# Performance work log

Measured on AMD Instinct MI355X. Metric: run time of the kernel, lower is better.

Reference implementation:

```python
import jax, jax.numpy as jnp
import numpy as np

N_NODES = 50000
N_EDGES = 1_600_000
FEAT, HIDDEN, NUM_CLASS = 128, 128, 64


def setup_inputs() -> dict:
    key = jax.random.key(0)
    k1, k2, k3, k4, k5 = jax.random.split(key, 5)
    h = jax.random.normal(k1, (N_NODES, FEAT), dtype=jnp.float32)
    edge_index = jax.random.randint(k2, (2, N_EDGES), 0, N_NODES, dtype=jnp.int32)
    # Glorot-ish init for the three GraphConv weights (bias=False)
    W1 = jax.random.normal(k3, (FEAT, HIDDEN), dtype=jnp.float32) * (1.0 / np.sqrt(FEAT))
    W2 = jax.random.normal(k4, (HIDDEN, HIDDEN), dtype=jnp.float32) * (1.0 / np.sqrt(HIDDEN))
    W3 = jax.random.normal(k5, (HIDDEN, NUM_CLASS), dtype=jnp.float32) * (1.0 / np.sqrt(HIDDEN))
    return {"h": h, "edge_index": edge_index, "W1": W1, "W2": W2, "W3": W3}


def _gcn_layer(h, W, src, dst, out_isqrt, in_isqrt, n_nodes):
    # DGL GraphConv, norm='both', bias=False: relu( D_in^{-1/2} A D_out^{-1/2} h W )
    h = h * out_isqrt[:, None]          # scale source features
    h = h @ W                            # dense projection (order-invariant)
    agg = jax.ops.segment_sum(h[src], dst, num_segments=n_nodes)  # SpMM aggregation
    agg = agg * in_isqrt[:, None]
    return jax.nn.relu(agg)


def reference(h, edge_index, W1, W2, W3):
    src, dst = edge_index[0], edge_index[1]
    ones = jnp.ones(src.shape[0], dtype=h.dtype)
    out_deg = jax.ops.segment_sum(ones, src, num_segments=N_NODES)
    in_deg = jax.ops.segment_sum(ones, dst, num_segments=N_NODES)
    out_isqrt = jnp.clip(out_deg, 1.0, None) ** -0.5
    in_isqrt = jnp.clip(in_deg, 1.0, None) ** -0.5
    h = _gcn_layer(h, W1, src, dst, out_isqrt, in_isqrt, N_NODES)
    h = _gcn_layer(h, W2, src, dst, out_isqrt, in_isqrt, N_NODES)
    h = _gcn_layer(h, W3, src, dst, out_isqrt, in_isqrt, N_NODES)
    return h
```

## Files before the change

kernel.cpp:

```cpp
#include <hip/hip_runtime.h>

#define N_NODES 50000
#define N_EDGES 1600000
#define FEAT 128
#define HIDDEN 128
#define NUM_CLASS 64

#define NBUCK 782
#define EPB 2048
#define NBLK 782
#define SCAP 2560
#define AGG_NBN 3125
#define GEMM_BLOCKS 782

#define HISTROW 50048
#define HISTW (HISTROW / 4)
#define NSHAD 128
#define HIST_EPB 12500

typedef _Float16 h8 __attribute__((ext_vector_type(8)));
typedef _Float16 h4 __attribute__((ext_vector_type(4)));
typedef float f32x4 __attribute__((ext_vector_type(4)));

__global__ __launch_bounds__(256) void passA_kernel(const int* __restrict__ ei,
                                                    unsigned* __restrict__ priv,
                                                    int* __restrict__ localoff,
                                                    int* __restrict__ Cmat) {
    __shared__ int cnt[1024];
    __shared__ int base[1024];
    __shared__ int cur[1024];
    __shared__ int tmp[256];
    __shared__ unsigned sorted[EPB];
    const int t = threadIdx.x;
    const int blk = blockIdx.x;
    for (int i = t; i < 1024; i += 256) cnt[i] = 0;
    __syncthreads();

    const int ebase = blk * EPB;
    unsigned packed[8];
    int bk[8];
#pragma unroll
    for (int j = 0; j < 8; ++j) {
        const int e = ebase + t + j * 256;
        if (e < N_EDGES) {
            const unsigned s = (unsigned)ei[e];
            const unsigned d = (unsigned)ei[N_EDGES + e];
            bk[j] = (int)(d >> 6);
            packed[j] = s | ((d & 63u) << 16) | ((d >> 6) << 22);
            atomicAdd(&cnt[bk[j]], 1);
        } else bk[j] = -1;
    }
    __syncthreads();

    const int c0 = cnt[4*t], c1 = cnt[4*t+1], c2 = cnt[4*t+2], c3 = cnt[4*t+3];
    const int s = c0 + c1 + c2 + c3;
    tmp[t] = s;
    __syncthreads();
    for (int off = 1; off < 256; off <<= 1) {
        int v = (t >= off) ? tmp[t - off] : 0;
        __syncthreads();
        tmp[t] += v;
        __syncthreads();
    }
    const int excl = tmp[t] - s;
    base[4*t] = excl;            cur[4*t] = excl;
    base[4*t+1] = excl+c0;       cur[4*t+1] = excl+c0;
    base[4*t+2] = excl+c0+c1;    cur[4*t+2] = excl+c0+c1;
    base[4*t+3] = excl+c0+c1+c2; cur[4*t+3] = excl+c0+c1+c2;
    __syncthreads();

    for (int b = t; b < NBUCK; b += 256) {
        localoff[(size_t)blk * NBUCK + b] = base[b];
        Cmat[(size_t)blk * NBUCK + b] = cnt[b];
    }
#pragma unroll
    for (int j = 0; j < 8; ++j)
        if (bk[j] >= 0) {
            const int pos = atomicAdd(&cur[bk[j]], 1);
            sorted[pos] = packed[j];
        }
    __syncthreads();
    const int total = min(EPB, N_EDGES - ebase);
    for (int i = t; i < total; i += 256) priv[(size_t)blk * EPB + i] = sorted[i];
}

__global__ __launch_bounds__(256) void hist8_kernel(const int* __restrict__ ei,
                                                    unsigned* __restrict__ hist8) {
    __shared__ unsigned hh[HISTW];
    const int t = threadIdx.x;
    for (int i = t; i < HISTW; i += 256) hh[i] = 0;
    __syncthreads();
    const int base = blockIdx.x * HIST_EPB;
    for (int j = t; j < HIST_EPB; j += 256) {
        const unsigned s = (unsigned)ei[base + j];
        atomicAdd(&hh[s >> 2], 1u << ((s & 3u) * 8u));
    }
    __syncthreads();
    unsigned* dst = hist8 + (size_t)blockIdx.x * HISTW;
    for (int i = t; i < HISTW; i += 256) dst[i] = hh[i];
}

__global__ __launch_bounds__(256) void scales8_kernel(const unsigned* __restrict__ hist8,
                                                      float* __restrict__ out_isqrt) {
    const int w = blockIdx.x * 256 + threadIdx.x;
    if (w >= HISTW) return;
    unsigned s0 = 0, s1 = 0, s2 = 0, s3 = 0;
    for (int b = 0; b < NSHAD; ++b) {
        const unsigned u = hist8[(size_t)b * HISTW + w];
        s0 += u & 255u; s1 += (u >> 8) & 255u; s2 += (u >> 16) & 255u; s3 += u >> 24;
    }
    const int n = w * 4;
    if (n < N_NODES)     out_isqrt[n]     = rsqrtf((float)(s0 < 1 ? 1 : s0));
    if (n + 1 < N_NODES) out_isqrt[n + 1] = rsqrtf((float)(s1 < 1 ? 1 : s1));
    if (n + 2 < N_NODES) out_isqrt[n + 2] = rsqrtf((float)(s2 < 1 ? 1 : s2));
    if (n + 3 < N_NODES) out_isqrt[n + 3] = rsqrtf((float)(s3 < 1 ? 1 : s3));
}

__global__ __launch_bounds__(256) void btotal_kernel(const int* __restrict__ Cmat,
                                                     int* __restrict__ total) {
    __shared__ int red[256];
    const int b = blockIdx.x;
    const int t = threadIdx.x;
    int s = 0;
    for (int blk = t; blk < NBLK; blk += 256) s += Cmat[(size_t)blk * NBUCK + b];
    red[t] = s;
    __syncthreads();
    for (int off = 128; off > 0; off >>= 1) {
        if (t < off) red[t] += red[t + off];
        __syncthreads();
    }
    if (t == 0) total[b] = red[0];
}

__global__ __launch_bounds__(256) void bscan2_kernel(const int* __restrict__ total,
                                                     int* __restrict__ csr_base,
                                                     int* __restrict__ row_off) {
    __shared__ int tt[1024];
    __shared__ int tmp[256];
    const int t = threadIdx.x;
    for (int i = t; i < 1024; i += 256) tt[i] = (i < NBUCK) ? total[i] : 0;
    __syncthreads();
    const int c0 = tt[4*t], c1 = tt[4*t+1], c2 = tt[4*t+2], c3 = tt[4*t+3];
    const int s = c0 + c1 + c2 + c3;
    tmp[t] = s;
    __syncthreads();
    for (int off = 1; off < 256; off <<= 1) {
        int v = (t >= off) ? tmp[t - off] : 0;
        __syncthreads();
        tmp[t] += v;
        __syncthreads();
    }
    const int excl = tmp[t] - s;
    if (4*t < NBUCK)   csr_base[4*t]   = excl;
    if (4*t+1 < NBUCK) csr_base[4*t+1] = excl + c0;
    if (4*t+2 < NBUCK) csr_base[4*t+2] = excl + c0 + c1;
    if (4*t+3 < NBUCK) csr_base[4*t+3] = excl + c0 + c1 + c2;
    if (t == 0) { csr_base[NBUCK] = N_EDGES; row_off[N_NODES] = N_EDGES; }
}

__global__ __launch_bounds__(256) void csr2_kernel(const int* __restrict__ localoff,
                                                   const unsigned* __restrict__ priv,
                                                   const int* __restrict__ csr_base,
                                                   unsigned short* __restrict__ csr,
                                                   int* __restrict__ row_off,
                                                   float* __restrict__ in_isqrt) {
    __shared__ unsigned gath[SCAP];
    __shared__ int tmp[256];
    __shared__ int cnt64[64];
    __shared__ int cur64[64];
    const int b = blockIdx.x;
    const int t = threadIdx.x;

    int off_[4], len_[4];
#pragma unroll
    for (int u = 0; u < 4; ++u) {
        const int blk = 4*t + u;
        if (blk < NBLK) {
            const int o = localoff[(size_t)blk * NBUCK + b];
            const int nxt = (b == NBUCK - 1) ? min(EPB, N_EDGES - blk * EPB)
                                             : localoff[(size_t)blk * NBUCK + b + 1];
            off_[u] = o; len_[u] = nxt - o;
        } else { off_[u] = 0; len_[u] = 0; }
    }
    const int s = len_[0] + len_[1] + len_[2] + len_[3];
    tmp[t] = s;
    __syncthreads();
    for (int off = 1; off < 256; off <<= 1) {
        int v = (t >= off) ? tmp[t - off] : 0;
        __syncthreads();
        tmp[t] += v;
        __syncthreads();
    }
    int run = tmp[t] - s;
    const int total = tmp[255];
#pragma unroll
    for (int u = 0; u < 4; ++u) {
        const int blk = 4*t + u;
        const unsigned* srcp = priv + (size_t)blk * EPB + off_[u];
        for (int j = 0; j < len_[u]; ++j)
            if (run + j < SCAP) gath[run + j] = srcp[j];
        run += len_[u];
    }
    if (t < 64) cnt64[t] = 0;
    __syncthreads();

    const int gtot = min(total, SCAP);
    for (int i = t; i < gtot; i += 256) atomicAdd(&cnt64[(gath[i] >> 16) & 63u], 1);
    __syncthreads();

    const int v64 = (t < 64) ? cnt64[t] : 0;
    tmp[t] = v64;
    __syncthreads();
    for (int off = 1; off < 64; off <<= 1) {
        int v = (t >= off) ? tmp[t - off] : 0;
        __syncthreads();
        tmp[t] += v;
        __syncthreads();
    }
    if (t < 64) {
        const int myoff = csr_base[b] + tmp[t] - v64;
        cur64[t] = myoff;
        const int node = b * 64 + t;
        if (node < N_NODES) {
            row_off[node] = myoff;
            in_isqrt[node] = rsqrtf((float)(v64 > 0 ? v64 : 1));
        }
    }
    __syncthreads();

    for (int i = t; i < gtot; i += 256) {
        const unsigned w = gath[i];
        const int pos = atomicAdd(&cur64[(w >> 16) & 63u], 1);
        csr[pos] = (unsigned short)(w & 0xFFFFu);
    }
}

__global__ __launch_bounds__(256) void wconv_kernel(const float* __restrict__ W1,
                                                    const float* __restrict__ W2,
                                                    const float* __restrict__ W3,
                                                    _Float16* __restrict__ WhT) {
    const int id = blockIdx.x * 256 + threadIdx.x;
    if (id < 16384) {
        const int n = id >> 7, k = id & 127;
        WhT[id] = (_Float16)W1[k * 128 + n];
    } else if (id < 32768) {
        const int i = id - 16384, n = i >> 7, k = i & 127;
        WhT[id] = (_Float16)W2[k * 128 + n];
    } else if (id < 40960) {
        const int i = id - 32768, n = i >> 7, k = i & 127;
        WhT[id] = (_Float16)W3[k * 64 + n];
    }
}

template <int OUT, typename InT>
__global__ __launch_bounds__(256) void gemm_kernel(const InT* __restrict__ H,
                                                   const _Float16* __restrict__ WhT,
                                                   const float* __restrict__ out_isqrt,
                                                   _Float16* __restrict__ Ys) {
    constexpr int NT = OUT / 16;
    __shared__ _Float16 Hs[64 * 128];
    char* hb = (char*)Hs;
    const int tid = threadIdx.x;
    const int bn = blockIdx.x * 64;

    {
        const int n = tid & 63, kg = tid >> 6;
        const int gn = bn + n;
        const int swz = (n & 7) << 4;
        if (gn < N_NODES) {
            if constexpr (sizeof(InT) == 4) {
                const float4* hrow = (const float4*)(H + (size_t)gn * FEAT) + kg * 8;
#pragma unroll
                for (int jj = 0; jj < 4; ++jj) {
                    const float4 u = hrow[jj * 2];
                    const float4 v = hrow[jj * 2 + 1];
                    h8 r;
                    r[0] = (_Float16)u.x; r[1] = (_Float16)u.y; r[2] = (_Float16)u.z; r[3] = (_Float16)u.w;
                    r[4] = (_Float16)v.x; r[5] = (_Float16)v.y; r[6] = (_Float16)v.z; r[7] = (_Float16)v.w;
                    *(h8*)(hb + ((n * 256 + kg * 64 + jj * 16) ^ swz)) = r;
                }
            } else {
                const h8* hrow = (const h8*)(H + (size_t)gn * FEAT) + kg * 4;
#pragma unroll
                for (int jj = 0; jj < 4; ++jj)
                    *(h8*)(hb + ((n * 256 + kg * 64 + jj * 16) ^ swz)) = hrow[jj];
            }
        } else {
            h8 z;
#pragma unroll
            for (int i = 0; i < 8; ++i) z[i] = (_Float16)0.f;
#pragma unroll
            for (int jj = 0; jj < 4; ++jj)
                *(h8*)(hb + ((n * 256 + kg * 64 + jj * 16) ^ swz)) = z;
        }
    }
    __syncthreads();

    const int l = tid & 63, w = tid >> 6;
    const int lm = l & 15, lk = l >> 4;
    const int nloc = w * 16 + lm;
    const int swzr = (nloc & 7) << 4;

    h8 bfrag[4];
#pragma unroll
    for (int kt = 0; kt < 4; ++kt)
        bfrag[kt] = *(const h8*)(hb + ((nloc * 256 + (lk * 8 + kt * 32) * 2) ^ swzr));

    f32x4 acc[NT];
#pragma unroll
    for (int nt = 0; nt < NT; ++nt) acc[nt] = (f32x4){0.f, 0.f, 0.f, 0.f};

#pragma unroll
    for (int nt = 0; nt < NT; ++nt) {
        const _Float16* wp = WhT + (size_t)(nt * 16 + lm) * 128 + lk * 8;
#pragma unroll
        for (int kt = 0; kt < 4; ++kt) {
            const h8 afrag = *(const h8*)(wp + kt * 32);
            acc[nt] = __builtin_amdgcn_mfma_f32_16x16x32_f16(afrag, bfrag[kt], acc[nt], 0, 0, 0);
        }
    }

    const int node = bn + w * 16 + lm;
    if (node < N_NODES) {
        const float sc = out_isqrt[node];
#pragma unroll
        for (int nt = 0; nt < NT; ++nt) {
            const int f0 = nt * 16 + lk * 4;
            h4 r;
            r[0] = (_Float16)(acc[nt][0] * sc);
            r[1] = (_Float16)(acc[nt][1] * sc);
            r[2] = (_Float16)(acc[nt][2] * sc);
            r[3] = (_Float16)(acc[nt][3] * sc);
            *(h4*)(Ys + ((size_t)(f0 >> 5) * N_NODES + node) * 32 + (f0 & 31)) = r;
        }
    }
}

template <int F, typename OT>
__global__ __launch_bounds__(256) void agg_kernel(const int* __restrict__ row_off,
                                                  const unsigned short* __restrict__ csr,
                                                  const _Float16* __restrict__ Ys,
                                                  const float* __restrict__ in_isqrt,
                                                  OT* __restrict__ out) {
    constexpr int NS = F / 32;
    const int s  = blockIdx.x & (NS - 1);
    const int nb = blockIdx.x / NS;
    const int tid = threadIdx.x;
    const int lane = tid & 63;
    const int j = lane >> 4;
    const int esub = (lane >> 2) & 3;
    const int q = lane & 3;

    const int d = nb * 16 + (tid >> 6) * 4 + j;
    const _Float16* Yp = Ys + (size_t)s * (N_NODES * 32) + q * 8;

    const int end = row_off[d + 1];
    float a0 = 0.f, a1 = 0.f, a2 = 0.f, a3 = 0.f, a4 = 0.f, a5 = 0.f, a6 = 0.f, a7 = 0.f;

    int e = row_off[d] + esub;
    for (; e + 12 < end; e += 16) {
        const int i0 = csr[e];
        const int i1 = csr[e + 4];
        const int i2 = csr[e + 8];
        const int i3 = csr[e + 12];
        const h8 v0 = *(const h8*)(Yp + (size_t)i0 * 32);
        const h8 v1 = *(const h8*)(Yp + (size_t)i1 * 32);
        const h8 v2 = *(const h8*)(Yp + (size_t)i2 * 32);
        const h8 v3 = *(const h8*)(Yp + (size_t)i3 * 32);
        a0 += (float)v0[0] + (float)v1[0] + (float)v2[0] + (float)v3[0];
        a1 += (float)v0[1] + (float)v1[1] + (float)v2[1] + (float)v3[1];
        a2 += (float)v0[2] + (float)v1[2] + (float)v2[2] + (float)v3[2];
        a3 += (float)v0[3] + (float)v1[3] + (float)v2[3] + (float)v3[3];
        a4 += (float)v0[4] + (float)v1[4] + (float)v2[4] + (float)v3[4];
        a5 += (float)v0[5] + (float)v1[5] + (float)v2[5] + (float)v3[5];
        a6 += (float)v0[6] + (float)v1[6] + (float)v2[6] + (float)v3[6];
        a7 += (float)v0[7] + (float)v1[7] + (float)v2[7] + (float)v3[7];
    }
    for (; e + 4 < end; e += 8) {
        const int i0 = csr[e];
        const int i1 = csr[e + 4];
        const h8 v0 = *(const h8*)(Yp + (size_t)i0 * 32);
        const h8 v1 = *(const h8*)(Yp + (size_t)i1 * 32);
        a0 += (float)v0[0] + (float)v1[0];
        a1 += (float)v0[1] + (float)v1[1];
        a2 += (float)v0[2] + (float)v1[2];
        a3 += (float)v0[3] + (float)v1[3];
        a4 += (float)v0[4] + (float)v1[4];
        a5 += (float)v0[5] + (float)v1[5];
        a6 += (float)v0[6] + (float)v1[6];
        a7 += (float)v0[7] + (float)v1[7];
    }
    if (e < end) {
        const int i0 = csr[e];
        const h8 v0 = *(const h8*)(Yp + (size_t)i0 * 32);
        a0 += (float)v0[0]; a1 += (float)v0[1]; a2 += (float)v0[2]; a3 += (float)v0[3];
        a4 += (float)v0[4]; a5 += (float)v0[5]; a6 += (float)v0[6]; a7 += (float)v0[7];
    }

    a0 += __shfl_xor(a0, 4, 64); a0 += __shfl_xor(a0, 8, 64);
    a1 += __shfl_xor(a1, 4, 64); a1 += __shfl_xor(a1, 8, 64);
    a2 += __shfl_xor(a2, 4, 64); a2 += __shfl_xor(a2, 8, 64);
    a3 += __shfl_xor(a3, 4, 64); a3 += __shfl_xor(a3, 8, 64);
    a4 += __shfl_xor(a4, 4, 64); a4 += __shfl_xor(a4, 8, 64);
    a5 += __shfl_xor(a5, 4, 64); a5 += __shfl_xor(a5, 8, 64);
    a6 += __shfl_xor(a6, 4, 64); a6 += __shfl_xor(a6, 8, 64);
    a7 += __shfl_xor(a7, 4, 64); a7 += __shfl_xor(a7, 8, 64);

    if (esub == 0) {
        const float isq = in_isqrt[d];
        const float r0 = fmaxf(a0 * isq, 0.f), r1 = fmaxf(a1 * isq, 0.f);
        const float r2 = fmaxf(a2 * isq, 0.f), r3 = fmaxf(a3 * isq, 0.f);
        const float r4 = fmaxf(a4 * isq, 0.f), r5 = fmaxf(a5 * isq, 0.f);
        const float r6 = fmaxf(a6 * isq, 0.f), r7 = fmaxf(a7 * isq, 0.f);
        if constexpr (sizeof(OT) == 2) {
            h8 o;
            o[0] = (_Float16)r0; o[1] = (_Float16)r1; o[2] = (_Float16)r2; o[3] = (_Float16)r3;
            o[4] = (_Float16)r4; o[5] = (_Float16)r5; o[6] = (_Float16)r6; o[7] = (_Float16)r7;
            *(h8*)((_Float16*)out + (size_t)d * F + s * 32 + q * 8) = o;
        } else {
            float* op = (float*)out + (size_t)d * F + s * 32 + q * 8;
            float4 w0 = {r0, r1, r2, r3}, w1 = {r4, r5, r6, r7};
            *(float4*)op = w0;
            *(float4*)(op + 4) = w1;
        }
    }
}

extern "C" void kernel_launch(void* const* d_in, const int* in_sizes, int n_in,
                              void* d_out, int out_size, void* d_ws, size_t ws_size,
                              hipStream_t stream) {
    const float* h  = (const float*)d_in[0];
    const int*   ei = (const int*)d_in[1];
    const float* W1 = (const float*)d_in[2];
    const float* W2 = (const float*)d_in[3];
    const float* W3 = (const float*)d_in[4];
    float* out = (float*)d_out;

    char* p = (char*)d_ws;
    auto alloc = [&p](size_t bytes) {
        void* r = (void*)p;
        p += (bytes + 255) & ~(size_t)255;
        return r;
    };
    int*   row_off  = (int*)alloc((N_NODES + 1) * sizeof(int));
    int*   csr_base = (int*)alloc((NBUCK + 1) * sizeof(int));
    int*   total    = (int*)alloc(NBUCK * sizeof(int));
    unsigned short* csr = (unsigned short*)alloc((size_t)N_EDGES * sizeof(unsigned short));
    float* in_isqrt  = (float*)alloc(N_NODES * sizeof(float));
    float* out_isqrt = (float*)alloc(N_NODES * sizeof(float));
    _Float16* WhT   = (_Float16*)alloc(40960 * sizeof(_Float16));
    _Float16* Ys    = (_Float16*)alloc((size_t)N_NODES * HIDDEN * sizeof(_Float16));
    _Float16* bufA  = (_Float16*)alloc((size_t)N_NODES * HIDDEN * sizeof(_Float16));
    _Float16* bufB  = (_Float16*)alloc((size_t)N_NODES * HIDDEN * sizeof(_Float16));
    unsigned* hist8 = (unsigned*)alloc((size_t)NSHAD * HISTW * sizeof(unsigned));
    unsigned* priv   = (unsigned*)bufA;
    int* localoff    = (int*)bufB;
    int* Cmat        = localoff + (size_t)NBLK * NBUCK;

    wconv_kernel<<<160, 256, 0, stream>>>(W1, W2, W3, WhT);
    passA_kernel<<<NBLK, 256, 0, stream>>>(ei, priv, localoff, Cmat);
    hist8_kernel<<<NSHAD, 256, 0, stream>>>(ei, hist8);
    btotal_kernel<<<NBUCK, 256, 0, stream>>>(Cmat, total);
    bscan2_kernel<<<1, 256, 0, stream>>>(total, csr_base, row_off);
    scales8_kernel<<<(HISTW + 255) / 256, 256, 0, stream>>>(hist8, out_isqrt);
    csr2_kernel<<<NBUCK, 256, 0, stream>>>(localoff, priv, csr_base, csr, row_off, in_isqrt);

    gemm_kernel<HIDDEN, float><<<GEMM_BLOCKS, 256, 0, stream>>>(h, WhT, out_isqrt, Ys);
    agg_kernel<HIDDEN, _Float16><<<4 * AGG_NBN, 256, 0, stream>>>(row_off, csr, Ys, in_isqrt, bufA);

    gemm_kernel<HIDDEN, _Float16><<<GEMM_BLOCKS, 256, 0, stream>>>(bufA, WhT + 16384, out_isqrt, Ys);
    agg_kernel<HIDDEN, _Float16><<<4 * AGG_NBN, 256, 0, stream>>>(row_off, csr, Ys, in_isqrt, bufB);

    gemm_kernel<NUM_CLASS, _Float16><<<GEMM_BLOCKS, 256, 0, stream>>>(bufB, WhT + 32768, out_isqrt, Ys);
    agg_kernel<NUM_CLASS, float><<<2 * AGG_NBN, 256, 0, stream>>>(row_off, csr, Ys, in_isqrt, out);
}
```

Measured before the change: 241.0 us.

## Fuse out-degree histogram into edge bucketing pass and merge setup kernels

The source-degree histogram now runs inside passA using per-block 4-bit nibble counters in shared memory. The separate hist8 kernel, and its second read of the edge sources, goes away. The reduction of those per-block histograms is folded into one setup kernel together with the weight transpose and fp16 conversion, and btotal now handles four buckets per block. This removes launches and one pass over the edge list. In exchange it writes and reads a larger per-block nibble histogram buffer, adds about 25KB of LDS to passA (lower occupancy), and assumes no node appears more than 15 times as a source within a 2048-edge chunk.

```diff
diff --git a/kernel.cpp b/kernel.cpp
--- a/kernel.cpp
+++ b/kernel.cpp
@@ -12,11 +12,7 @@
 #define SCAP 2560
 #define AGG_NBN 3125
 #define GEMM_BLOCKS 782
-
-#define HISTROW 50048
-#define HISTW (HISTROW / 4)
-#define NSHAD 128
-#define HIST_EPB 12500
+#define NSHW 6256
 
 typedef _Float16 h8 __attribute__((ext_vector_type(8)));
 typedef _Float16 h4 __attribute__((ext_vector_type(4)));
@@ -25,15 +21,18 @@
 __global__ __launch_bounds__(256) void passA_kernel(const int* __restrict__ ei,
                                                     unsigned* __restrict__ priv,
                                                     int* __restrict__ localoff,
-                                                    int* __restrict__ Cmat) {
+                                                    int* __restrict__ Cmat,
+                                                    unsigned* __restrict__ nibshad) {
     __shared__ int cnt[1024];
     __shared__ int base[1024];
     __shared__ int cur[1024];
     __shared__ int tmp[256];
     __shared__ unsigned sorted[EPB];
+    __shared__ unsigned nib[NSHW];
     const int t = threadIdx.x;
     const int blk = blockIdx.x;
     for (int i = t; i < 1024; i += 256) cnt[i] = 0;
+    for (int i = t; i < NSHW; i += 256) nib[i] = 0;
     __syncthreads();
 
     const int ebase = blk * EPB;
@@ -48,6 +47,7 @@
             bk[j] = (int)(d >> 6);
             packed[j] = s | ((d & 63u) << 16) | ((d >> 6) << 22);
             atomicAdd(&cnt[bk[j]], 1);
+            atomicAdd(&nib[s >> 3], 1u << ((s & 7u) * 4u));
         } else bk[j] = -1;
     }
     __syncthreads();
@@ -82,54 +82,26 @@
     __syncthreads();
     const int total = min(EPB, N_EDGES - ebase);
     for (int i = t; i < total; i += 256) priv[(size_t)blk * EPB + i] = sorted[i];
-}
-
-__global__ __launch_bounds__(256) void hist8_kernel(const int* __restrict__ ei,
-                                                    unsigned* __restrict__ hist8) {
-    __shared__ unsigned hh[HISTW];
-    const int t = threadIdx.x;
-    for (int i = t; i < HISTW; i += 256) hh[i] = 0;
-    __syncthreads();
-    const int base = blockIdx.x * HIST_EPB;
-    for (int j = t; j < HIST_EPB; j += 256) {
-        const unsigned s = (unsigned)ei[base + j];
-        atomicAdd(&hh[s >> 2], 1u << ((s & 3u) * 8u));
-    }
-    __syncthreads();
-    unsigned* dst = hist8 + (size_t)blockIdx.x * HISTW;
-    for (int i = t; i < HISTW; i += 256) dst[i] = hh[i];
-}
-
-__global__ __launch_bounds__(256) void scales8_kernel(const unsigned* __restrict__ hist8,
-                                                      float* __restrict__ out_isqrt) {
-    const int w = blockIdx.x * 256 + threadIdx.x;
-    if (w >= HISTW) return;
-    unsigned s0 = 0, s1 = 0, s2 = 0, s3 = 0;
-    for (int b = 0; b < NSHAD; ++b) {
-        const unsigned u = hist8[(size_t)b * HISTW + w];
-        s0 += u & 255u; s1 += (u >> 8) & 255u; s2 += (u >> 16) & 255u; s3 += u >> 24;
-    }
-    const int n = w * 4;
-    if (n < N_NODES)     out_isqrt[n]     = rsqrtf((float)(s0 < 1 ? 1 : s0));
-    if (n + 1 < N_NODES) out_isqrt[n + 1] = rsqrtf((float)(s1 < 1 ? 1 : s1));
-    if (n + 2 < N_NODES) out_isqrt[n + 2] = rsqrtf((float)(s2 < 1 ? 1 : s2));
-    if (n + 3 < N_NODES) out_isqrt[n + 3] = rsqrtf((float)(s3 < 1 ? 1 : s3));
+    unsigned* dst = nibshad + (size_t)blk * NSHW;
+    for (int i = t; i < NSHW; i += 256) dst[i] = nib[i];
 }
 
 __global__ __launch_bounds__(256) void btotal_kernel(const int* __restrict__ Cmat,
                                                      int* __restrict__ total) {
+    const int b0 = blockIdx.x * 4;
+    const int t = threadIdx.x;
+    const int c = t & 3, r = t >> 2;
+    int s = 0;
+    if (b0 + c < NBUCK)
+        for (int i = r; i < NBLK; i += 64) s += Cmat[(size_t)i * NBUCK + b0 + c];
     __shared__ int red[256];
-    const int b = blockIdx.x;
-    const int t = threadIdx.x;
-    int s = 0;
-    for (int blk = t; blk < NBLK; blk += 256) s += Cmat[(size_t)blk * NBUCK + b];
     red[t] = s;
     __syncthreads();
-    for (int off = 128; off > 0; off >>= 1) {
+    for (int off = 128; off >= 4; off >>= 1) {
         if (t < off) red[t] += red[t + off];
         __syncthreads();
     }
-    if (t == 0) total[b] = red[0];
+    if (t < 4 && b0 + t < NBUCK) total[b0 + t] = red[t];
 }
 
 __global__ __launch_bounds__(256) void bscan2_kernel(const int* __restrict__ total,
@@ -156,6 +128,60 @@
     if (4*t+2 < NBUCK) csr_base[4*t+2] = excl + c0 + c1;
     if (4*t+3 < NBUCK) csr_base[4*t+3] = excl + c0 + c1 + c2;
     if (t == 0) { csr_base[NBUCK] = N_EDGES; row_off[N_NODES] = N_EDGES; }
+}
+
+__global__ __launch_bounds__(256) void setup_kernel(const float* __restrict__ W1,
+                                                    const float* __restrict__ W2,
+                                                    const float* __restrict__ W3,
+                                                    _Float16* __restrict__ WhT,
+                                                    const unsigned* __restrict__ nibshad,
+                                                    float* __restrict__ out_isqrt) {
+    const int bid = blockIdx.x;
+    const int t = threadIdx.x;
+    if (bid < 160) {
+        const int id = bid * 256 + t;
+        if (id < 16384) {
+            const int n = id >> 7, k = id & 127;
+            WhT[id] = (_Float16)W1[k * 128 + n];
+        } else if (id < 32768) {
+            const int i = id - 16384, n = i >> 7, k = i & 127;
+            WhT[id] = (_Float16)W2[k * 128 + n];
+        } else if (id < 40960) {
+            const int i = id - 32768, n = i >> 7, k = i & 127;
+            WhT[id] = (_Float16)W3[k * 64 + n];
+        }
+        return;
+    }
+    const int blk = bid - 160;
+    const int w0 = blk * 8;
+    const int wl = t & 7, c = t >> 3;
+    int acc[8] = {0, 0, 0, 0, 0, 0, 0, 0};
+    for (int sh = c; sh < NBLK; sh += 32) {
+        const unsigned u = nibshad[(size_t)sh * NSHW + w0 + wl];
+        acc[0] += u & 15u;         acc[1] += (u >> 4) & 15u;
+        acc[2] += (u >> 8) & 15u;  acc[3] += (u >> 12) & 15u;
+        acc[4] += (u >> 16) & 15u; acc[5] += (u >> 20) & 15u;
+        acc[6] += (u >> 24) & 15u; acc[7] += (u >> 28);
+    }
+    __shared__ int red[32][8][8];
+#pragma unroll
+    for (int nb = 0; nb < 8; ++nb) red[c][wl][nb] = acc[nb];
+    __syncthreads();
+    for (int off = 16; off > 0; off >>= 1) {
+        if (c < off) {
+#pragma unroll
+            for (int nb = 0; nb < 8; ++nb) red[c][wl][nb] += red[c + off][wl][nb];
+        }
+        __syncthreads();
+    }
+    if (t < 64) {
+        const int wl2 = t >> 3, nb = t & 7;
+        const int node = (w0 + wl2) * 8 + nb;
+        if (node < N_NODES) {
+            const int d = red[0][wl2][nb];
+            out_isqrt[node] = rsqrtf((float)(d < 1 ? 1 : d));
+        }
+    }
 }
 
 __global__ __launch_bounds__(256) void csr2_kernel(const int* __restrict__ localoff,
@@ -232,23 +258,6 @@
         const unsigned w = gath[i];
         const int pos = atomicAdd(&cur64[(w >> 16) & 63u], 1);
         csr[pos] = (unsigned short)(w & 0xFFFFu);
-    }
-}
-
-__global__ __launch_bounds__(256) void wconv_kernel(const float* __restrict__ W1,
-                                                    const float* __restrict__ W2,
-                                                    const float* __restrict__ W3,
-                                                    _Float16* __restrict__ WhT) {
-    const int id = blockIdx.x * 256 + threadIdx.x;
-    if (id < 16384) {
-        const int n = id >> 7, k = id & 127;
-        WhT[id] = (_Float16)W1[k * 128 + n];
-    } else if (id < 32768) {
-        const int i = id - 16384, n = i >> 7, k = i & 127;
-        WhT[id] = (_Float16)W2[k * 128 + n];
-    } else if (id < 40960) {
-        const int i = id - 32768, n = i >> 7, k = i & 127;
-        WhT[id] = (_Float16)W3[k * 64 + n];
     }
 }
 
@@ -452,17 +461,15 @@
     _Float16* Ys    = (_Float16*)alloc((size_t)N_NODES * HIDDEN * sizeof(_Float16));
     _Float16* bufA  = (_Float16*)alloc((size_t)N_NODES * HIDDEN * sizeof(_Float16));
     _Float16* bufB  = (_Float16*)alloc((size_t)N_NODES * HIDDEN * sizeof(_Float16));
-    unsigned* hist8 = (unsigned*)alloc((size_t)NSHAD * HISTW * sizeof(unsigned));
+    unsigned* nibshad = (unsigned*)alloc((size_t)NBLK * NSHW * sizeof(unsigned));
     unsigned* priv   = (unsigned*)bufA;
     int* localoff    = (int*)bufB;
     int* Cmat        = localoff + (size_t)NBLK * NBUCK;
 
-    wconv_kernel<<<160, 256, 0, stream>>>(W1, W2, W3, WhT);
-    passA_kernel<<<NBLK, 256, 0, stream>>>(ei, priv, localoff, Cmat);
-    hist8_kernel<<<NSHAD, 256, 0, stream>>>(ei, hist8);
-    btotal_kernel<<<NBUCK, 256, 0, stream>>>(Cmat, total);
+    passA_kernel<<<NBLK, 256, 0, stream>>>(ei, priv, localoff, Cmat, nibshad);
+    btotal_kernel<<<(NBUCK + 3) / 4, 256, 0, stream>>>(Cmat, total);
     bscan2_kernel<<<1, 256, 0, stream>>>(total, csr_base, row_off);
-    scales8_kernel<<<(HISTW + 255) / 256, 256, 0, stream>>>(hist8, out_isqrt);
+    setup_kernel<<<160 + NBLK, 256, 0, stream>>>(W1, W2, W3, WhT, nibshad, out_isqrt);
     csr2_kernel<<<NBUCK, 256, 0, stream>>>(localoff, priv, csr_base, csr, row_off, in_isqrt);
 
     gemm_kernel<HIDDEN, float><<<GEMM_BLOCKS, 256, 0, stream>>>(h, WhT, out_isqrt, Ys);
```

Result: faster. 235.2 us (-2.4%).
